# Optimization experiments

Measured on AMD Instinct MI355X. Metric: run time of the kernel, lower is better.

## Reference

```python
import jax, jax.numpy as jnp
import numpy as np

B, S, H = 2, 1024, 2048
NH, NKV, HD = 32, 8, 64          # head_dim = H // NH
G = NH // NKV                    # GQA group size = 4
THETA = 500000.0
EPS = 1e-5
SCALE = HD ** -0.5


def _rope_neox(x, positions):
    # x: [B, S, n_heads, HD]; neox style: rotate concatenated halves
    inv_freq = 1.0 / (THETA ** (jnp.arange(0, HD, 2, dtype=jnp.float32) / HD))  # [HD/2]
    ang = positions[..., None].astype(jnp.float32) * inv_freq                    # [B, S, HD/2]
    cos = jnp.cos(ang)[:, :, None, :]
    sin = jnp.sin(ang)[:, :, None, :]
    x1, x2 = jnp.split(x, 2, axis=-1)
    return jnp.concatenate([x1 * cos - x2 * sin, x2 * cos + x1 * sin], axis=-1)


def setup_inputs() -> dict:
    key = jax.random.key(0)
    k1, k2, k3 = jax.random.split(key, 3)
    hidden_states = jax.random.normal(k1, (B, S, H), jnp.float32)
    w_qkv = jax.random.normal(k2, ((NH + 2 * NKV) * HD, H), jnp.float32) * 0.02
    w_o = jax.random.normal(k3, (H, NH * HD), jnp.float32) * 0.02
    norm_w = jnp.ones((H,), jnp.float32)
    positions = jnp.broadcast_to(jnp.arange(S, dtype=jnp.int32), (B, S))
    return {"hidden_states": hidden_states, "positions": positions,
            "w_qkv": w_qkv, "w_o": w_o, "norm_w": norm_w}


def reference(hidden_states, positions, w_qkv, w_o, norm_w):
    # QKV projection (bias=False) and split
    qkv = hidden_states @ w_qkv.T                                 # [B,S,3072]
    q, k, v = jnp.split(qkv, [NH * HD, NH * HD + NKV * HD], axis=-1)
    q = q.reshape(B, S, NH, HD)
    k = k.reshape(B, S, NKV, HD)
    v = v.reshape(B, S, NKV, HD)

    # RoPE on q and k (full rotary_dim = head_dim)
    q = _rope_neox(q, positions)
    k = _rope_neox(k, positions)

    # Causal GQA attention (dense-prefill equivalent of RadixAttention)
    qg = q.reshape(B, S, NKV, G, HD)
    scores = jnp.einsum('bqhgd,bkhd->bhgqk', qg, k) * SCALE       # [B,NKV,G,S,S]
    causal = jnp.tril(jnp.ones((S, S), dtype=bool))
    scores = jnp.where(causal, scores, jnp.float32(-1e30))
    probs = jax.nn.softmax(scores, axis=-1)
    attn = jnp.einsum('bhgqk,bkhd->bqhgd', probs, v).reshape(B, S, NH * HD)

    # BitNet sub-norm (RMSNorm) then output projection
    var = jnp.mean(attn * attn, axis=-1, keepdims=True)
    normed = attn * jax.lax.rsqrt(var + EPS) * norm_w
    return normed @ w_o.T                                         # [B,S,H]
```

## Files before the change

kernel.cpp:

```cpp
#include <hip/hip_runtime.h>
#include <hip/hip_bf16.h>
#include <cstdint>
#include <cstddef>

typedef __bf16 bf16;
typedef __bf16 bf16x2 __attribute__((ext_vector_type(2)));
typedef __bf16 bf16x4 __attribute__((ext_vector_type(4)));
typedef __bf16 bf16x8 __attribute__((ext_vector_type(8)));
typedef float  f32x4  __attribute__((ext_vector_type(4)));

__device__ __forceinline__ void async_copy16(const void* g, void* l) {
  __builtin_amdgcn_global_load_lds((const __attribute__((address_space(1))) void*)g,
                                   (__attribute__((address_space(3))) void*)l,
                                   16, 0, 0);
}

__device__ __forceinline__ int swz(int row) { return ((row >> 1) & 3) << 3; }

__device__ __forceinline__ bool block_flag_is_f32(const unsigned int* w, int tid,
                                                  int* sflag) {
  if (tid < 64) {
    int weird = 0;
#pragma unroll
    for (int c = 0; c < 2; ++c) {
      const unsigned int lo = w[c * 64 + tid] & 0xffffu;
      const unsigned int ex = (lo >> 7) & 0xffu;
      if (ex >= 134u) ++weird;
    }
    const unsigned long long m1 = __ballot(weird >= 1);
    const unsigned long long m2 = __ballot(weird == 2);
    if (tid == 0) *sflag = (__popcll(m1) + __popcll(m2) >= 8) ? 1 : 0;
  }
  __syncthreads();
  return *sflag != 0;
}

__global__ __launch_bounds__(256) void convert_all(
    const void* __restrict__ s0, const void* __restrict__ s1,
    const void* __restrict__ s2, const void* __restrict__ s3,
    bf16* __restrict__ d0, bf16* __restrict__ d1, bf16* __restrict__ d2,
    float* __restrict__ ssum) {
  __shared__ int sflag;
  const int tid = threadIdx.x;
  const bool f32 = block_flag_is_f32((const unsigned int*)s0, tid, &sflag);
  if (blockIdx.x == 0) {
    ((float4*)ssum)[tid * 2]     = make_float4(0.f, 0.f, 0.f, 0.f);
    ((float4*)ssum)[tid * 2 + 1] = make_float4(0.f, 0.f, 0.f, 0.f);
  }
#pragma unroll
  for (int k = 0; k < 4; ++k) {
    const int i = blockIdx.x * 256 + tid + k * 917504;
    const void* src; bf16* dst; int off; bool fold = false;
    if      (i < 1048576) { src = s0; dst = d0; off = i; }
    else if (i < 2621440) { src = s1; dst = d1; off = i - 1048576; }
    else                  { src = s2; dst = d2; off = i - 2621440; fold = true; }
    float v[4];
    if (f32) {
      const float4 t = ((const float4*)src)[off];
      v[0] = t.x; v[1] = t.y; v[2] = t.z; v[3] = t.w;
    } else {
      const bf16x4 t = ((const bf16x4*)src)[off];
#pragma unroll
      for (int j = 0; j < 4; ++j) v[j] = (float)t[j];
    }
    if (fold) {
      const int k0 = (off * 4) & 2047;
#pragma unroll
      for (int j = 0; j < 4; ++j) {
        const float w = f32 ? ((const float*)s3)[k0 + j] : (float)((const bf16*)s3)[k0 + j];
        v[j] *= w;
      }
    }
    bf16x4 o;
#pragma unroll
    for (int j = 0; j < 4; ++j) o[j] = (bf16)v[j];
    *(bf16x4*)(dst + (size_t)off * 4) = o;
  }
}

__global__ __launch_bounds__(256) void gemm_qkv_rope(
    const bf16* __restrict__ A, const bf16* __restrict__ B,
    const int* __restrict__ pos,
    bf16* __restrict__ Q, bf16* __restrict__ K, bf16* __restrict__ V)
{
  __shared__ __align__(16) bf16 As[2][2 * 64 * 32];
  __shared__ __align__(16) bf16 Bs[2][2 * 128 * 32];
  const int tid = threadIdx.x, wave = tid >> 6, lane = tid & 63;
  const int l15 = lane & 15, l4 = lane >> 4;
  const int bid = blockIdx.x;
  const int sid = (bid & 7) * 96 + (bid >> 3);
  const int m0 = (sid & 31) * 64, n0 = (sid >> 5) * 128;
  const int wm = (wave >> 1) * 32, wn = (wave & 1) * 64;
  const int swz_ro = (l4 * 8) ^ swz(l15);

  f32x4 acc[2][4] = {};

  auto stage = [&](int buf, int kt) {
#pragma unroll
    for (int c = 0; c < 2; ++c) {
      const int e = c * 2048 + tid * 8;
      const int kc = e >> 11, row = (e >> 5) & 63;
      const int o = (e & 31) ^ swz(row);
      async_copy16(A + (size_t)(m0 + row) * 2048 + kt + kc * 32 + o, &As[buf][e]);
    }
#pragma unroll
    for (int c = 0; c < 4; ++c) {
      const int e = c * 2048 + tid * 8;
      const int kc = e >> 12, row = (e >> 5) & 127;
      const int o = (e & 31) ^ swz(row);
      async_copy16(B + (size_t)(n0 + row) * 2048 + kt + kc * 32 + o, &Bs[buf][e]);
    }
  };

  stage(0, 0);
  __syncthreads();
  int cur = 0;
  for (int kt = 0; kt < 2048; kt += 64) {
    if (kt + 64 < 2048) stage(cur ^ 1, kt + 64);
#pragma unroll
    for (int s = 0; s < 2; ++s) {
      bf16x8 af[2], bfr[4];
#pragma unroll
      for (int i = 0; i < 2; ++i)
        af[i] = *(const bf16x8*)(&As[cur][s * 2048 + (wm + i * 16 + l15) * 32 + swz_ro]);
#pragma unroll
      for (int j = 0; j < 4; ++j)
        bfr[j] = *(const bf16x8*)(&Bs[cur][s * 4096 + (wn + j * 16 + l15) * 32 + swz_ro]);
#pragma unroll
      for (int i = 0; i < 2; ++i)
#pragma unroll
        for (int j = 0; j < 4; ++j)
          acc[i][j] = __builtin_amdgcn_mfma_f32_16x16x32_bf16(af[i], bfr[j], acc[i][j], 0, 0, 0);
    }
    __syncthreads();
    cur ^= 1;
  }

  if (n0 < 2560) {
    const bool isQ = (n0 < 2048);
#pragma unroll
    for (int i = 0; i < 2; ++i)
#pragma unroll
      for (int j = 0; j < 4; ++j) {
        const int col = n0 + wn + j * 16 + l15;
        const int hd = isQ ? col : (col - 2048);
        const int hh = hd >> 6, d = hd & 63;
        const int fi = d & 31;
        const float ifr = __expf((float)fi * -0.41007385554f);
#pragma unroll
        for (int r = 0; r < 4; ++r) {
          const int m = m0 + wm + i * 16 + l4 * 4 + r;
          const int b = m >> 10, s = m & 1023;
          const float ang = (float)pos[m] * ifr;
          float sn, cs;
          __sincosf(ang, &sn, &cs);
          const float x  = acc[i][j][r];
          const float xp = acc[i][j ^ 2][r];
          const float v = (d < 32) ? (x * cs - xp * sn) : (x * cs + xp * sn);
          if (isQ) Q[(((size_t)(b * 32 + hh)) * 1024 + s) * 64 + d] = (bf16)(v * 0.125f);
          else     K[(((size_t)(b * 8 + hh)) * 1024 + s) * 64 + d] = (bf16)v;
        }
      }
  } else {
#pragma unroll
    for (int i = 0; i < 2; ++i)
#pragma unroll
      for (int j = 0; j < 4; ++j) {
        const int cv = n0 + wn + j * 16 + l15 - 2560;
        const int hh = cv >> 6, d = cv & 63;
#pragma unroll
        for (int r = 0; r < 4; ++r) {
          const int m = m0 + wm + i * 16 + l4 * 4 + r;
          const int b = m >> 10, s = m & 1023;
          const int sp = (s & ~31) + ((s & 15) * 2 + ((s >> 4) & 1));
          V[(((size_t)(b * 8 + hh)) * 64 + d) * 1024 + sp] = (bf16)acc[i][j][r];
        }
      }
  }
}

__global__ __launch_bounds__(256) void attn_kernel(
    const bf16* __restrict__ Q, const bf16* __restrict__ K,
    const bf16* __restrict__ Vt, bf16* __restrict__ O, float* __restrict__ ssum)
{
  __shared__ __align__(16) bf16 Ks[2 * 128 * 32];
  __shared__ __align__(16) bf16 Vs[4 * 64 * 32];
  __shared__ __align__(16) bf16 Ps[4 * 128 * 40];

  const int tid = threadIdx.x, wave = tid >> 6, lane = tid & 63;
  const int l15 = lane & 15, l4 = lane >> 4;
  const int swz_ro = (l4 * 8) ^ swz(l15);
  const int ip = blockIdx.x, bh = blockIdx.y;
  const int b = bh >> 5, h = bh & 31, kvh = h >> 2;
  const int qlo = ip * 64, qhi = (15 - ip) * 64;
  const bf16* Qb = Q + ((size_t)(b * 32 + h)) * 65536;
  const bf16* Kb = K + ((size_t)(b * 8 + kvh)) * 65536;
  const bf16* Vb = Vt + ((size_t)(b * 8 + kvh)) * 65536;

#pragma unroll
  for (int c = 0; c < 4; ++c) {
    const int e = c * 2048 + tid * 8;
    const int dchunk = e >> 12;
    const int row = (e & 4095) >> 5;
    const int qb = (row < 64) ? qlo : qhi;
    const int o = (e & 31) ^ swz(row);
    async_copy16(Qb + (size_t)(qb + (row & 63)) * 64 + dchunk * 32 + o, Ps + e);
  }
  __syncthreads();
  bf16x8 aq[2][2];
#pragma unroll
  for (int i = 0; i < 2; ++i)
#pragma unroll
    for (int s = 0; s < 2; ++s)
      aq[i][s] = *(const bf16x8*)(Ps + s * 4096 + (i * 64 + wave * 16 + l15) * 32 + swz_ro);
  __syncthreads();

  float m_s[2][4], l_s[2][4];
  f32x4 o_acc[2][4] = {};
#pragma unroll
  for (int i = 0; i < 2; ++i)
#pragma unroll
    for (int r = 0; r < 4; ++r) { m_s[i][r] = -3.0e4f; l_s[i][r] = 0.f; }

  const int nkt = (1151 - 64 * ip) >> 7;
  for (int kt = 0; kt < nkt; ++kt) {
    const int k0 = kt * 128;
    const bool lo_act = (k0 < (ip + 1) * 64);
#pragma unroll
    for (int c = 0; c < 4; ++c) {
      const int e = c * 2048 + tid * 8;
      const int krow = (e & 4095) >> 5;
      const int ko = (e & 31) ^ swz(krow);
      async_copy16(Kb + (size_t)(k0 + krow) * 64 + (e >> 12) * 32 + ko, Ks + e);
      const int drow = (e & 2047) >> 5;
      const int vo = (e & 31) ^ swz(drow);
      async_copy16(Vb + (size_t)drow * 1024 + k0 + (e >> 11) * 32 + vo, Vs + e);
    }
    __syncthreads();

    f32x4 sc[2][8] = {};
#pragma unroll
    for (int j = 0; j < 8; ++j) {
      const bf16x8 bk0 = *(const bf16x8*)(Ks + (j * 16 + l15) * 32 + swz_ro);
      const bf16x8 bk1 = *(const bf16x8*)(Ks + 4096 + (j * 16 + l15) * 32 + swz_ro);
      sc[1][j] = __builtin_amdgcn_mfma_f32_16x16x32_bf16(aq[1][0], bk0, sc[1][j], 0, 0, 0);
      sc[1][j] = __builtin_amdgcn_mfma_f32_16x16x32_bf16(aq[1][1], bk1, sc[1][j], 0, 0, 0);
      if (lo_act) {
        sc[0][j] = __builtin_amdgcn_mfma_f32_16x16x32_bf16(aq[0][0], bk0, sc[0][j], 0, 0, 0);
        sc[0][j] = __builtin_amdgcn_mfma_f32_16x16x32_bf16(aq[0][1], bk1, sc[0][j], 0, 0, 0);
      }
    }

#pragma unroll
    for (int hh = 0; hh < 2; ++hh) {
      if (hh == 0 && !lo_act) continue;
      const int qb = hh ? qhi : qlo;
#pragma unroll
      for (int r = 0; r < 4; ++r) {
        const int rl = wave * 16 + l4 * 4 + r;
        const int rg = qb + rl;
        float mx = -3.0e4f;
#pragma unroll
        for (int j = 0; j < 8; ++j) {
          float v = sc[hh][j][r];
          if (k0 + j * 16 + l15 > rg) v = -3.0e4f;
          sc[hh][j][r] = v;
          mx = fmaxf(mx, v);
        }
#pragma unroll
        for (int off = 1; off < 16; off <<= 1) mx = fmaxf(mx, __shfl_xor(mx, off));
        const float mnew = fmaxf(m_s[hh][r], mx);
        const float alpha = __expf(m_s[hh][r] - mnew);
        m_s[hh][r] = mnew;
        float rs = 0.f;
#pragma unroll
        for (int t = 0; t < 4; ++t) {
          const float pv0 = __expf(sc[hh][2 * t][r]     - mnew);
          const float pv1 = __expf(sc[hh][2 * t + 1][r] - mnew);
          rs += pv0 + pv1;
          bf16x2 pk; pk[0] = (bf16)pv0; pk[1] = (bf16)pv1;
          *(bf16x2*)(Ps + t * 5120 + (hh * 64 + rl) * 40 + l15 * 2) = pk;
        }
#pragma unroll
        for (int off = 1; off < 16; off <<= 1) rs += __shfl_xor(rs, off);
        l_s[hh][r] = l_s[hh][r] * alpha + rs;
#pragma unroll
        for (int jd = 0; jd < 4; ++jd) o_acc[hh][jd][r] *= alpha;
      }
    }

#pragma unroll
    for (int ks = 0; ks < 4; ++ks) {
      bf16x8 bv[4];
#pragma unroll
      for (int jd = 0; jd < 4; ++jd)
        bv[jd] = *(const bf16x8*)(Vs + ks * 2048 + (jd * 16 + l15) * 32 + swz_ro);
#pragma unroll
      for (int hh = 0; hh < 2; ++hh) {
        if (hh == 0 && !lo_act) continue;
        const bf16x8 ap = *(const bf16x8*)(Ps + ks * 5120 + (hh * 64 + wave * 16 + l15) * 40 + l4 * 8);
#pragma unroll
        for (int jd = 0; jd < 4; ++jd)
          o_acc[hh][jd] = __builtin_amdgcn_mfma_f32_16x16x32_bf16(ap, bv[jd], o_acc[hh][jd], 0, 0, 0);
      }
    }
    __syncthreads();
  }

#pragma unroll
  for (int hh = 0; hh < 2; ++hh) {
    const int qb = hh ? qhi : qlo;
#pragma unroll
    for (int r = 0; r < 4; ++r) {
      const float inv = 1.0f / l_s[hh][r];
      const int srow = qb + wave * 16 + l4 * 4 + r;
      bf16* op = O + ((size_t)(b * 1024 + srow)) * 2048 + h * 64;
      float ss = 0.f;
#pragma unroll
      for (int jd = 0; jd < 4; ++jd) {
        const float v = o_acc[hh][jd][r] * inv;
        op[jd * 16 + l15] = (bf16)v;
        ss += v * v;
      }
#pragma unroll
      for (int off = 1; off < 16; off <<= 1) ss += __shfl_xor(ss, off);
      if (l15 == 0) atomicAdd(&ssum[b * 1024 + srow], ss);
    }
  }
}

__global__ __launch_bounds__(256) void gemm_out(
    const bf16* __restrict__ A, const bf16* __restrict__ B,
    const float* __restrict__ ssum, const unsigned int* __restrict__ hs_raw,
    void* __restrict__ out)
{
  __shared__ __align__(16) bf16 As[4 * 64 * 32];
  __shared__ __align__(16) bf16 Bs[4 * 128 * 32];
  __shared__ int sflag;
  const int tid = threadIdx.x, wave = tid >> 6, lane = tid & 63;
  const bool f32out = block_flag_is_f32(hs_raw, tid, &sflag);
  const int l15 = lane & 15, l4 = lane >> 4;
  const int bid = blockIdx.x;
  const int sid = (bid & 7) * 64 + (bid >> 3);
  const int m0 = (sid & 31) * 64, n0 = (sid >> 5) * 128;
  const int wm = (wave >> 1) * 32, wn = (wave & 1) * 64;
  const int KD = 2048;
  const int swz_ro = (l4 * 8) ^ swz(l15);

  f32x4 acc[2][4] = {};

  for (int kt = 0; kt < KD; kt += 128) {
#pragma unroll
    for (int c = 0; c < 4; ++c) {
      const int e = c * 2048 + tid * 8;
      const int kc = e >> 11, row = (e >> 5) & 63;
      const int o = (e & 31) ^ swz(row);
      async_copy16(A + (size_t)(m0 + row) * KD + kt + kc * 32 + o, As + e);
    }
#pragma unroll
    for (int c = 0; c < 8; ++c) {
      const int e = c * 2048 + tid * 8;
      const int kc = e >> 12, row = (e >> 5) & 127;
      const int o = (e & 31) ^ swz(row);
      async_copy16(B + (size_t)(n0 + row) * KD + kt + kc * 32 + o, Bs + e);
    }
    __syncthreads();
#pragma unroll
    for (int s = 0; s < 4; ++s) {
      bf16x8 af[2], bfr[4];
#pragma unroll
      for (int i = 0; i < 2; ++i)
        af[i] = *(const bf16x8*)(As + s * 2048 + (wm + i * 16 + l15) * 32 + swz_ro);
#pragma unroll
      for (int j = 0; j < 4; ++j)
        bfr[j] = *(const bf16x8*)(Bs + s * 4096 + (wn + j * 16 + l15) * 32 + swz_ro);
#pragma unroll
      for (int i = 0; i < 2; ++i)
#pragma unroll
        for (int j = 0; j < 4; ++j)
          acc[i][j] = __builtin_amdgcn_mfma_f32_16x16x32_bf16(af[i], bfr[j], acc[i][j], 0, 0, 0);
    }
    __syncthreads();
  }

#pragma unroll
  for (int i = 0; i < 2; ++i)
#pragma unroll
    for (int r = 0; r < 4; ++r) {
      const int row = m0 + wm + i * 16 + l4 * 4 + r;
      const float ri = rsqrtf(ssum[row] * (1.0f / 2048.0f) + 1e-5f);
#pragma unroll
      for (int j = 0; j < 4; ++j) {
        const int col = n0 + wn + j * 16 + l15;
        const size_t idx = (size_t)row * 2048 + col;
        const float v = ri * acc[i][j][r];
        if (f32out) ((float*)out)[idx] = v;
        else        ((bf16*)out)[idx]  = (bf16)v;
      }
    }
}

extern "C" void kernel_launch(void* const* d_in, const int* in_sizes, int n_in,
                              void* d_out, int out_size, void* d_ws, size_t ws_size,
                              hipStream_t stream) {
  const void* hs     = d_in[0];
  const int*  pos    = (const int*)d_in[1];
  const void* w_qkv  = d_in[2];
  const void* w_o    = d_in[3];
  const void* norm_w = d_in[4];

  char* ws = (char*)d_ws;
  bf16*  hs_b   = (bf16*) (ws);
  bf16*  wqkv_b = (bf16*) (ws + 8388608);
  bf16*  w_o_b  = (bf16*) (ws + 20971520);
  float* ssum   = (float*)(ws + 29360128);
  bf16*  Qr     = (bf16*) (ws + 29368320);
  bf16*  Kr     = (bf16*) (ws + 37756928);
  bf16*  Vtr    = (bf16*) (ws + 39854080);
  bf16*  attn_o = (bf16*) (ws + 41951232);

  convert_all<<<3584, 256, 0, stream>>>(hs, w_qkv, w_o, norm_w,
                                        hs_b, wqkv_b, w_o_b, ssum);
  gemm_qkv_rope<<<768, 256, 0, stream>>>(hs_b, wqkv_b, pos, Qr, Kr, Vtr);
  attn_kernel<<<dim3(8, 64), 256, 0, stream>>>(Qr, Kr, Vtr, attn_o, ssum);
  gemm_out<<<512, 256, 0, stream>>>(attn_o, w_o_b, ssum,
                                    (const unsigned int*)hs, d_out);
}
```

Baseline: 206.7 us.

## Fuse fp32-to-bf16 conversion into GEMM loaders and fold norm weight into attention

```diff
diff --git a/kernel.cpp b/kernel.cpp
--- a/kernel.cpp
+++ b/kernel.cpp
@@ -35,88 +35,83 @@
   return *sflag != 0;
 }
 
-__global__ __launch_bounds__(256) void convert_all(
-    const void* __restrict__ s0, const void* __restrict__ s1,
-    const void* __restrict__ s2, const void* __restrict__ s3,
-    bf16* __restrict__ d0, bf16* __restrict__ d1, bf16* __restrict__ d2,
-    float* __restrict__ ssum) {
-  __shared__ int sflag;
-  const int tid = threadIdx.x;
-  const bool f32 = block_flag_is_f32((const unsigned int*)s0, tid, &sflag);
-  if (blockIdx.x == 0) {
-    ((float4*)ssum)[tid * 2]     = make_float4(0.f, 0.f, 0.f, 0.f);
-    ((float4*)ssum)[tid * 2 + 1] = make_float4(0.f, 0.f, 0.f, 0.f);
-  }
-#pragma unroll
-  for (int k = 0; k < 4; ++k) {
-    const int i = blockIdx.x * 256 + tid + k * 917504;
-    const void* src; bf16* dst; int off; bool fold = false;
-    if      (i < 1048576) { src = s0; dst = d0; off = i; }
-    else if (i < 2621440) { src = s1; dst = d1; off = i - 1048576; }
-    else                  { src = s2; dst = d2; off = i - 2621440; fold = true; }
-    float v[4];
-    if (f32) {
-      const float4 t = ((const float4*)src)[off];
-      v[0] = t.x; v[1] = t.y; v[2] = t.z; v[3] = t.w;
-    } else {
-      const bf16x4 t = ((const bf16x4*)src)[off];
-#pragma unroll
-      for (int j = 0; j < 4; ++j) v[j] = (float)t[j];
-    }
-    if (fold) {
-      const int k0 = (off * 4) & 2047;
-#pragma unroll
-      for (int j = 0; j < 4; ++j) {
-        const float w = f32 ? ((const float*)s3)[k0 + j] : (float)((const bf16*)s3)[k0 + j];
-        v[j] *= w;
-      }
-    }
-    bf16x4 o;
-#pragma unroll
-    for (int j = 0; j < 4; ++j) o[j] = (bf16)v[j];
-    *(bf16x4*)(dst + (size_t)off * 4) = o;
-  }
-}
-
 __global__ __launch_bounds__(256) void gemm_qkv_rope(
-    const bf16* __restrict__ A, const bf16* __restrict__ B,
+    const void* __restrict__ Araw, const void* __restrict__ Braw,
     const int* __restrict__ pos,
-    bf16* __restrict__ Q, bf16* __restrict__ K, bf16* __restrict__ V)
+    bf16* __restrict__ Q, bf16* __restrict__ K, bf16* __restrict__ V,
+    float* __restrict__ ssum)
 {
   __shared__ __align__(16) bf16 As[2][2 * 64 * 32];
   __shared__ __align__(16) bf16 Bs[2][2 * 128 * 32];
+  __shared__ int sflag;
   const int tid = threadIdx.x, wave = tid >> 6, lane = tid & 63;
+  const bool f32 = block_flag_is_f32((const unsigned int*)Araw, tid, &sflag);
   const int l15 = lane & 15, l4 = lane >> 4;
   const int bid = blockIdx.x;
+  if (bid == 0) {
+    ((float4*)ssum)[tid * 2]     = make_float4(0.f, 0.f, 0.f, 0.f);
+    ((float4*)ssum)[tid * 2 + 1] = make_float4(0.f, 0.f, 0.f, 0.f);
+  }
   const int sid = (bid & 7) * 96 + (bid >> 3);
   const int m0 = (sid & 31) * 64, n0 = (sid >> 5) * 128;
   const int wm = (wave >> 1) * 32, wn = (wave & 1) * 64;
   const int swz_ro = (l4 * 8) ^ swz(l15);
 
+  const int arow = tid >> 2, aseg = (tid & 3) * 16;
+  const int brow = tid >> 1, bseg = (tid & 1) * 32;
+  float4 a_ld[4], b_ld[8];
+
+  auto stage_load = [&](int kt) {
+    const size_t aoff = (size_t)(m0 + arow) * 2048 + kt + aseg;
+    const size_t boff = (size_t)(n0 + brow) * 2048 + kt + bseg;
+    if (f32) {
+      const float4* Ap = (const float4*)Araw + (aoff >> 2);
+      const float4* Bp = (const float4*)Braw + (boff >> 2);
+#pragma unroll
+      for (int c = 0; c < 4; ++c) a_ld[c] = Ap[c];
+#pragma unroll
+      for (int c = 0; c < 8; ++c) b_ld[c] = Bp[c];
+    } else {
+      const float4* Ap = (const float4*)Araw + (aoff >> 3);
+      const float4* Bp = (const float4*)Braw + (boff >> 3);
+#pragma unroll
+      for (int c = 0; c < 2; ++c) a_ld[c] = Ap[c];
+#pragma unroll
+      for (int c = 0; c < 4; ++c) b_ld[c] = Bp[c];
+    }
+  };
+  auto cvt_write = [&](int buf) {
+    const int akc = aseg >> 5, ab = aseg & 31;
+    const int bkc = bseg >> 5;
+#pragma unroll
+    for (int blk = 0; blk < 2; ++blk) {
+      bf16x8 w;
+      if (f32) {
+#pragma unroll
+        for (int j = 0; j < 8; ++j) w[j] = (bf16)((&a_ld[blk * 2].x)[j]);
+      } else w = *(const bf16x8*)&a_ld[blk];
+      *(bf16x8*)(&As[buf][akc * 2048 + arow * 32 + ((ab + blk * 8) ^ swz(arow))]) = w;
+    }
+#pragma unroll
+    for (int blk = 0; blk < 4; ++blk) {
+      bf16x8 w;
+      if (f32) {
+#pragma unroll
+        for (int j = 0; j < 8; ++j) w[j] = (bf16)((&b_ld[blk * 2].x)[j]);
+      } else w = *(const bf16x8*)&b_ld[blk];
+      *(bf16x8*)(&Bs[buf][bkc * 4096 + brow * 32 + ((blk * 8) ^ swz(brow))]) = w;
+    }
+  };
+
   f32x4 acc[2][4] = {};
 
-  auto stage = [&](int buf, int kt) {
-#pragma unroll
-    for (int c = 0; c < 2; ++c) {
-      const int e = c * 2048 + tid * 8;
-      const int kc = e >> 11, row = (e >> 5) & 63;
-      const int o = (e & 31) ^ swz(row);
-      async_copy16(A + (size_t)(m0 + row) * 2048 + kt + kc * 32 + o, &As[buf][e]);
-    }
-#pragma unroll
-    for (int c = 0; c < 4; ++c) {
-      const int e = c * 2048 + tid * 8;
-      const int kc = e >> 12, row = (e >> 5) & 127;
-      const int o = (e & 31) ^ swz(row);
-      async_copy16(B + (size_t)(n0 + row) * 2048 + kt + kc * 32 + o, &Bs[buf][e]);
-    }
-  };
-
-  stage(0, 0);
+  stage_load(0);
+  cvt_write(0);
   __syncthreads();
   int cur = 0;
   for (int kt = 0; kt < 2048; kt += 64) {
-    if (kt + 64 < 2048) stage(cur ^ 1, kt + 64);
+    const bool has_next = (kt + 64 < 2048);
+    if (has_next) stage_load(kt + 64);
 #pragma unroll
     for (int s = 0; s < 2; ++s) {
       bf16x8 af[2], bfr[4];
@@ -132,6 +127,7 @@
         for (int j = 0; j < 4; ++j)
           acc[i][j] = __builtin_amdgcn_mfma_f32_16x16x32_bf16(af[i], bfr[j], acc[i][j], 0, 0, 0);
     }
+    if (has_next) cvt_write(cur ^ 1);
     __syncthreads();
     cur ^= 1;
   }
@@ -181,13 +177,17 @@
 
 __global__ __launch_bounds__(256) void attn_kernel(
     const bf16* __restrict__ Q, const bf16* __restrict__ K,
-    const bf16* __restrict__ Vt, bf16* __restrict__ O, float* __restrict__ ssum)
+    const bf16* __restrict__ Vt, const void* __restrict__ norm_w,
+    const unsigned int* __restrict__ hs_raw,
+    bf16* __restrict__ O, float* __restrict__ ssum)
 {
   __shared__ __align__(16) bf16 Ks[2 * 128 * 32];
   __shared__ __align__(16) bf16 Vs[4 * 64 * 32];
   __shared__ __align__(16) bf16 Ps[4 * 128 * 40];
+  __shared__ int sflag;
 
   const int tid = threadIdx.x, wave = tid >> 6, lane = tid & 63;
+  const bool f32 = block_flag_is_f32(hs_raw, tid, &sflag);
   const int l15 = lane & 15, l4 = lane >> 4;
   const int swz_ro = (l4 * 8) ^ swz(l15);
   const int ip = blockIdx.x, bh = blockIdx.y;
@@ -197,6 +197,12 @@
   const bf16* Kb = K + ((size_t)(b * 8 + kvh)) * 65536;
   const bf16* Vb = Vt + ((size_t)(b * 8 + kvh)) * 65536;
 
+  float nw[4];
+#pragma unroll
+  for (int jd = 0; jd < 4; ++jd)
+    nw[jd] = f32 ? ((const float*)norm_w)[h * 64 + jd * 16 + l15]
+                 : (float)((const bf16*)norm_w)[h * 64 + jd * 16 + l15];
+
 #pragma unroll
   for (int c = 0; c < 4; ++c) {
     const int e = c * 2048 + tid * 8;
@@ -319,7 +325,7 @@
 #pragma unroll
       for (int jd = 0; jd < 4; ++jd) {
         const float v = o_acc[hh][jd][r] * inv;
-        op[jd * 16 + l15] = (bf16)v;
+        op[jd * 16 + l15] = (bf16)(v * nw[jd]);
         ss += v * v;
       }
 #pragma unroll
@@ -330,57 +336,87 @@
 }
 
 __global__ __launch_bounds__(256) void gemm_out(
-    const bf16* __restrict__ A, const bf16* __restrict__ B,
+    const bf16* __restrict__ A, const void* __restrict__ Braw,
     const float* __restrict__ ssum, const unsigned int* __restrict__ hs_raw,
     void* __restrict__ out)
 {
-  __shared__ __align__(16) bf16 As[4 * 64 * 32];
-  __shared__ __align__(16) bf16 Bs[4 * 128 * 32];
+  __shared__ __align__(16) bf16 As[2][2 * 64 * 32];
+  __shared__ __align__(16) bf16 Bs[2][2 * 128 * 32];
   __shared__ int sflag;
   const int tid = threadIdx.x, wave = tid >> 6, lane = tid & 63;
-  const bool f32out = block_flag_is_f32(hs_raw, tid, &sflag);
+  const bool f32 = block_flag_is_f32(hs_raw, tid, &sflag);
   const int l15 = lane & 15, l4 = lane >> 4;
   const int bid = blockIdx.x;
   const int sid = (bid & 7) * 64 + (bid >> 3);
   const int m0 = (sid & 31) * 64, n0 = (sid >> 5) * 128;
   const int wm = (wave >> 1) * 32, wn = (wave & 1) * 64;
-  const int KD = 2048;
   const int swz_ro = (l4 * 8) ^ swz(l15);
 
-  f32x4 acc[2][4] = {};
-
-  for (int kt = 0; kt < KD; kt += 128) {
-#pragma unroll
-    for (int c = 0; c < 4; ++c) {
+  const int brow = tid >> 1, bseg = (tid & 1) * 32;
+  float4 b_ld[8];
+
+  auto stage_A = [&](int buf, int kt) {
+#pragma unroll
+    for (int c = 0; c < 2; ++c) {
       const int e = c * 2048 + tid * 8;
       const int kc = e >> 11, row = (e >> 5) & 63;
       const int o = (e & 31) ^ swz(row);
-      async_copy16(A + (size_t)(m0 + row) * KD + kt + kc * 32 + o, As + e);
-    }
-#pragma unroll
-    for (int c = 0; c < 8; ++c) {
-      const int e = c * 2048 + tid * 8;
-      const int kc = e >> 12, row = (e >> 5) & 127;
-      const int o = (e & 31) ^ swz(row);
-      async_copy16(B + (size_t)(n0 + row) * KD + kt + kc * 32 + o, Bs + e);
-    }
-    __syncthreads();
-#pragma unroll
-    for (int s = 0; s < 4; ++s) {
+      async_copy16(A + (size_t)(m0 + row) * 2048 + kt + kc * 32 + o, &As[buf][e]);
+    }
+  };
+  auto stage_loadB = [&](int kt) {
+    const size_t boff = (size_t)(n0 + brow) * 2048 + kt + bseg;
+    if (f32) {
+      const float4* Bp = (const float4*)Braw + (boff >> 2);
+#pragma unroll
+      for (int c = 0; c < 8; ++c) b_ld[c] = Bp[c];
+    } else {
+      const float4* Bp = (const float4*)Braw + (boff >> 3);
+#pragma unroll
+      for (int c = 0; c < 4; ++c) b_ld[c] = Bp[c];
+    }
+  };
+  auto cvt_writeB = [&](int buf) {
+    const int bkc = bseg >> 5;
+#pragma unroll
+    for (int blk = 0; blk < 4; ++blk) {
+      bf16x8 w;
+      if (f32) {
+#pragma unroll
+        for (int j = 0; j < 8; ++j) w[j] = (bf16)((&b_ld[blk * 2].x)[j]);
+      } else w = *(const bf16x8*)&b_ld[blk];
+      *(bf16x8*)(&Bs[buf][bkc * 4096 + brow * 32 + ((blk * 8) ^ swz(brow))]) = w;
+    }
+  };
+
+  f32x4 acc[2][4] = {};
+
+  stage_A(0, 0);
+  stage_loadB(0);
+  cvt_writeB(0);
+  __syncthreads();
+  int cur = 0;
+  for (int kt = 0; kt < 2048; kt += 64) {
+    const bool has_next = (kt + 64 < 2048);
+    if (has_next) { stage_A(cur ^ 1, kt + 64); stage_loadB(kt + 64); }
+#pragma unroll
+    for (int s = 0; s < 2; ++s) {
       bf16x8 af[2], bfr[4];
 #pragma unroll
       for (int i = 0; i < 2; ++i)
-        af[i] = *(const bf16x8*)(As + s * 2048 + (wm + i * 16 + l15) * 32 + swz_ro);
+        af[i] = *(const bf16x8*)(&As[cur][s * 2048 + (wm + i * 16 + l15) * 32 + swz_ro]);
 #pragma unroll
       for (int j = 0; j < 4; ++j)
-        bfr[j] = *(const bf16x8*)(Bs + s * 4096 + (wn + j * 16 + l15) * 32 + swz_ro);
+        bfr[j] = *(const bf16x8*)(&Bs[cur][s * 4096 + (wn + j * 16 + l15) * 32 + swz_ro]);
 #pragma unroll
       for (int i = 0; i < 2; ++i)
 #pragma unroll
         for (int j = 0; j < 4; ++j)
           acc[i][j] = __builtin_amdgcn_mfma_f32_16x16x32_bf16(af[i], bfr[j], acc[i][j], 0, 0, 0);
     }
+    if (has_next) cvt_writeB(cur ^ 1);
     __syncthreads();
+    cur ^= 1;
   }
 
 #pragma unroll
@@ -394,8 +430,8 @@
         const int col = n0 + wn + j * 16 + l15;
         const size_t idx = (size_t)row * 2048 + col;
         const float v = ri * acc[i][j][r];
-        if (f32out) ((float*)out)[idx] = v;
-        else        ((bf16*)out)[idx]  = (bf16)v;
+        if (f32) ((float*)out)[idx] = v;
+        else     ((bf16*)out)[idx]  = (bf16)v;
       }
     }
 }
@@ -410,19 +446,16 @@
   const void* norm_w = d_in[4];
 
   char* ws = (char*)d_ws;
-  bf16*  hs_b   = (bf16*) (ws);
-  bf16*  wqkv_b = (bf16*) (ws + 8388608);
-  bf16*  w_o_b  = (bf16*) (ws + 20971520);
-  float* ssum   = (float*)(ws + 29360128);
-  bf16*  Qr     = (bf16*) (ws + 29368320);
-  bf16*  Kr     = (bf16*) (ws + 37756928);
-  bf16*  Vtr    = (bf16*) (ws + 39854080);
-  bf16*  attn_o = (bf16*) (ws + 41951232);
-
-  convert_all<<<3584, 256, 0, stream>>>(hs, w_qkv, w_o, norm_w,
-                                        hs_b, wqkv_b, w_o_b, ssum);
-  gemm_qkv_rope<<<768, 256, 0, stream>>>(hs_b, wqkv_b, pos, Qr, Kr, Vtr);
-  attn_kernel<<<dim3(8, 64), 256, 0, stream>>>(Qr, Kr, Vtr, attn_o, ssum);
-  gemm_out<<<512, 256, 0, stream>>>(attn_o, w_o_b, ssum,
+  float* ssum   = (float*)(ws);
+  bf16*  Qr     = (bf16*) (ws + 8192);
+  bf16*  Kr     = (bf16*) (ws + 8396800);
+  bf16*  Vtr    = (bf16*) (ws + 10493952);
+  bf16*  attn_o = (bf16*) (ws + 12591104);
+
+  gemm_qkv_rope<<<768, 256, 0, stream>>>(hs, w_qkv, pos, Qr, Kr, Vtr, ssum);
+  attn_kernel<<<dim3(8, 64), 256, 0, stream>>>(Qr, Kr, Vtr, norm_w,
+                                               (const unsigned int*)hs,
+                                               attn_o, ssum);
+  gemm_out<<<512, 256, 0, stream>>>(attn_o, w_o, ssum,
                                     (const unsigned int*)hs, d_out);
 }
```

After: 452.4 us. 119% more time.
